# Optimization experiments

Measured on AMD Instinct MI355X. Metric: run time of the kernel, lower is better.

Reference implementation:

```python
import jax, jax.numpy as jnp
import numpy as np
import math

EPS = 1e-12


def _cmul(ar, ai, br, bi):
    return ar * br - ai * bi, ar * bi + ai * br


def _wilson_seed(x):
    # x: (B, 4, L, L) -> conj of canonical Wilson-line path, (B, L, L) re/im
    ux_r, ux_i, uy_r, uy_i = x[:, 0], x[:, 1], x[:, 2], x[:, 3]
    B, L, _ = ux_r.shape
    dt = x.dtype

    def step(c, u):
        cr, ci = c
        ur, ui = u
        nr, ni = _cmul(cr, ci, ur, ui)
        return (nr, ni), (nr, ni)

    # cumulative complex product along x at y=0
    init_r = jnp.ones((B,), dt)
    init_i = jnp.zeros((B,), dt)
    xs = (ux_r[:, :-1, 0].T, ux_i[:, :-1, 0].T)  # (L-1, B)
    _, (axr, axi) = jax.lax.scan(step, (init_r, init_i), xs)
    x_axis_r = jnp.concatenate([init_r[None], axr], 0).T  # (B, L)
    x_axis_i = jnp.concatenate([init_i[None], axi], 0).T

    # cumulative complex product along y, vectorized over x
    ys = (jnp.moveaxis(uy_r[:, :, :-1], 2, 0), jnp.moveaxis(uy_i[:, :, :-1], 2, 0))  # (L-1, B, L)
    _, (pr, pi_) = jax.lax.scan(step, (x_axis_r, x_axis_i), ys)
    path_r = jnp.moveaxis(jnp.concatenate([x_axis_r[None], pr], 0), 0, 2)  # (B, L, L)
    path_i = jnp.moveaxis(jnp.concatenate([x_axis_i[None], pi_], 0), 0, 2)
    return path_r, -path_i  # conjugate


def _wrap(t):
    return (t + math.pi) % (2.0 * math.pi) - math.pi


def _initial_features(x):
    seed_r, seed_i = _wilson_seed(x)
    ax = jnp.arctan2(x[:, 1], x[:, 0])
    ay = jnp.arctan2(x[:, 3], x[:, 2])
    plaq = _wrap(ax + jnp.roll(ay, -1, axis=1) - jnp.roll(ax, -1, axis=2) - ay)
    pc = jnp.cos(plaq)
    pavg = (pc + jnp.roll(pc, 1, 1) + jnp.roll(pc, -1, 1)
            + jnp.roll(pc, 1, 2) + jnp.roll(pc, -1, 2)) / 5.0
    scalars = jnp.stack([jnp.ones_like(pc), pc, pavg], axis=1)  # (B, 3, L, L)
    return seed_r[:, None] * scalars, seed_i[:, None] * scalars


def _transport_fwd(fr, fi, x, mu):
    lr, li = (x[:, 0], x[:, 1]) if mu == 0 else (x[:, 2], x[:, 3])
    sr = jnp.roll(fr, -1, axis=mu + 2)
    si = jnp.roll(fi, -1, axis=mu + 2)
    return _cmul(lr[:, None], li[:, None], sr, si)


def _transport_bwd(fr, fi, x, mu):
    lr, li = (x[:, 0], x[:, 1]) if mu == 0 else (x[:, 2], x[:, 3])
    cr = jnp.roll(lr, 1, axis=mu + 1)
    ci = jnp.roll(-li, 1, axis=mu + 1)
    sr = jnp.roll(fr, 1, axis=mu + 2)
    si = jnp.roll(fi, 1, axis=mu + 2)
    return _cmul(cr[:, None], ci[:, None], sr, si)


def _lconv(fr, fi, x, center, fwd_w, bwd_w):
    out_r = jnp.einsum('oi,bixy->boxy', center, fr)
    out_i = jnp.einsum('oi,bixy->boxy', center, fi)
    for mu in range(2):
        fr2, fi2 = _transport_fwd(fr, fi, x, mu)
        br2, bi2 = _transport_bwd(fr, fi, x, mu)
        out_r = out_r + jnp.einsum('oi,bixy->boxy', fwd_w[mu], fr2) \
                      + jnp.einsum('oi,bixy->boxy', bwd_w[mu], br2)
        out_i = out_i + jnp.einsum('oi,bixy->boxy', fwd_w[mu], fi2) \
                      + jnp.einsum('oi,bixy->boxy', bwd_w[mu], bi2)
    return out_r, out_i


def _modrelu(fr, fi, bias):
    mag = jnp.sqrt(fr * fr + fi * fi + EPS)
    act = jax.nn.relu(mag + bias[None, :, None, None])
    scale = act / jnp.maximum(mag, EPS)
    return fr * scale, fi * scale


def setup_inputs() -> dict:
    key = jax.random.key(0)
    ks = jax.random.split(key, 11)
    B, L, H, O = 64, 128, 16, 8
    s = 0.1
    return {
        'x': jax.random.normal(ks[0], (B, 4, L, L), jnp.float32),
        'center1': s * jax.random.normal(ks[1], (H, 3), jnp.float32),
        'fwd_w1': s * jax.random.normal(ks[2], (2, H, 3), jnp.float32),
        'bwd_w1': s * jax.random.normal(ks[3], (2, H, 3), jnp.float32),
        'bias1': jnp.zeros((H,), jnp.float32),
        'center2': s * jax.random.normal(ks[4], (O, H), jnp.float32),
        'fwd_w2': s * jax.random.normal(ks[5], (2, O, H), jnp.float32),
        'bwd_w2': s * jax.random.normal(ks[6], (2, O, H), jnp.float32),
        'bias2': jnp.zeros((O,), jnp.float32),
        'ro_weight': s * jax.random.normal(ks[7], (O,), jnp.float32),
        'ro_bias': jnp.zeros((1,), jnp.float32),
    }


def reference(x, center1, fwd_w1, bwd_w1, bias1, center2, fwd_w2, bwd_w2, bias2, ro_weight, ro_bias):
    fr, fi = _initial_features(x)
    fr, fi = _lconv(fr, fi, x, center1, fwd_w1, bwd_w1)
    fr, fi = _modrelu(fr, fi, bias1)
    fr, fi = _lconv(fr, fi, x, center2, fwd_w2, bwd_w2)
    fr, fi = _modrelu(fr, fi, bias2)
    inv = fr * fr + fi * fi
    return jnp.einsum('c,bcxy->bxy', ro_weight, inv)[:, None] + ro_bias.reshape(1, 1, 1, 1)
```

## Files before the change

### kernel.cpp

```cpp
#include <hip/hip_runtime.h>
#include <math.h>

#define LQ   128
#define BQ   64
#define LL   (LQ*LQ)
#define H1   16
#define O2   8
#define TILE 16
#define REG  18
#define NPTS (REG*REG)
#define PCR  22
#define PCN  (PCR*PCR)
#define LKR  23
#define LKN  (LKR*LKR)
#define SDR  20
#define SDN  (SDR*SDR)
#define FSTR 10

typedef float f2 __attribute__((ext_vector_type(2)));
using bf8 = __attribute__((ext_vector_type(8))) short;
using f4  = __attribute__((ext_vector_type(4))) float;

__device__ __forceinline__ int wrapi(int v) { return v & (LQ - 1); }

__device__ __forceinline__ unsigned pack_bf(float hi, float lo) {
    return __builtin_amdgcn_perm(__float_as_uint(hi), __float_as_uint(lo),
                                 0x07060302u);
}

#define WS_W1 ((size_t)BQ * LL)

__global__ __launch_bounds__(256)
void k_scan(const float* __restrict__ x,
            const float* __restrict__ c1, const float* __restrict__ fw1,
            const float* __restrict__ bw1, float* __restrict__ ws) {
    int blk = blockIdx.x;
    if (blk == BQ * 8) {
        int tid = threadIdx.x;
        if (tid < 120) {
            int t = tid / 24, r = tid - t * 24;
            int c = r >> 3, op = r & 7;
            const float* src = (t == 0) ? c1 : (t == 1) ? fw1 : (t == 2) ? bw1
                             : (t == 3) ? (fw1 + 48) : (bw1 + 48);
            float2 v = make_float2(src[(2 * op) * 3 + c], src[(2 * op + 1) * 3 + c]);
            ((float2*)ws)[WS_W1 + tid] = v;
        }
        return;
    }
    int b = blk >> 3, rq = blk & 7;
    int l = threadIdx.x & 63, w = threadIdx.x >> 6;
    const float* x0 = x + (size_t)b * 4 * LL;
    const float* x1 = x0 + LL;

    float ur0 = x0[(2 * l) * LQ],     ui0 = x1[(2 * l) * LQ];
    float ur1 = x0[(2 * l + 1) * LQ], ui1 = x1[(2 * l + 1) * LQ];
    float pr = ur0 * ur1 - ui0 * ui1;
    float pi = ur0 * ui1 + ui0 * ur1;
    for (int d = 1; d < 64; d <<= 1) {
        float qr = __shfl_up(pr, d, 64);
        float qi = __shfl_up(pi, d, 64);
        if (l >= d) {
            float nr = qr * pr - qi * pi;
            float ni = qr * pi + qi * pr;
            pr = nr; pi = ni;
        }
    }
    float er = __shfl_up(pr, 1, 64);
    float ei = __shfl_up(pi, 1, 64);
    if (l == 0) { er = 1.f; ei = 0.f; }
    float e1r = er * ur0 - ei * ui0;
    float e1i = er * ui0 + ei * ur0;

    const float* yrp = x + (size_t)(b * 4 + 2) * LL;
    const float* yip = yrp + LL;
    float4* seed4 = (float4*)ws;

    for (int k = 0; k < 4; ++k) {
        int i = rq * 16 + w * 4 + k;
        float cxr = __shfl((i & 1) ? e1r : er, i >> 1, 64);
        float cxi = __shfl((i & 1) ? e1i : ei, i >> 1, 64);
        const float* yr = yrp + (size_t)i * LQ;
        const float* yi = yip + (size_t)i * LQ;
        float vr0 = yr[2 * l],     vi0 = yi[2 * l];
        float vr1 = yr[2 * l + 1], vi1 = yi[2 * l + 1];
        float sr = vr0 * vr1 - vi0 * vi1;
        float si = vr0 * vi1 + vi0 * vr1;
        for (int d = 1; d < 64; d <<= 1) {
            float qr = __shfl_up(sr, d, 64);
            float qi = __shfl_up(si, d, 64);
            if (l >= d) {
                float nr = qr * sr - qi * si;
                float ni = qr * si + qi * sr;
                sr = nr; si = ni;
            }
        }
        float gr = __shfl_up(sr, 1, 64);
        float gi = __shfl_up(si, 1, 64);
        if (l == 0) { gr = 1.f; gi = 0.f; }
        float s0r = cxr * gr - cxi * gi;
        float s0i = cxr * gi + cxi * gr;
        float s1r = s0r * vr0 - s0i * vi0;
        float s1i = s0r * vi0 + s0i * vr0;
        seed4[((size_t)b * LL + (size_t)i * LQ) / 2 + l] =
            make_float4(s0r, -s0i, s1r, -s1i);
    }
}

__global__ __launch_bounds__(256, 4)
void k_main(const float* __restrict__ x,
            const float* __restrict__ c2, const float* __restrict__ fw2,
            const float* __restrict__ bw2, const float* __restrict__ b1,
            const float* __restrict__ b2,
            const float* __restrict__ ro, const float* __restrict__ rob,
            const float* __restrict__ ws, float* __restrict__ out) {
    __shared__ unsigned s_f1r[NPTS * FSTR];
    __shared__ unsigned s_f1i[NPTS * FSTR];
    __shared__ f2 s_ux[LKN];
    __shared__ f2 s_uy[LKN];
    __shared__ float s_pc[PCN];
    __shared__ f2 s_sd[SDN];
    int tid = threadIdx.x;
    int b = blockIdx.z, i0 = blockIdx.y * TILE, j0 = blockIdx.x * TILE;
    const float* x0 = x + (size_t)b * 4 * LL;
    const float* x1 = x0 + LL;
    const float* x2 = x0 + 2 * LL;
    const float* x3 = x0 + 3 * LL;
    const float2* seed = (const float2*)ws + (size_t)b * LL;
    const float2* W1 = (const float2*)ws + WS_W1;

    bool z1 = true;
#pragma unroll
    for (int h = 0; h < H1; ++h) z1 = z1 && (b1[h] == 0.f);
    bool z2 = true;
#pragma unroll
    for (int o = 0; o < O2; ++o) z2 = z2 && (b2[o] == 0.f);

    for (int p = tid; p < LKN; p += 256) {
        int ri = p / LKR, rj = p - ri * LKR;
        int gi = wrapi(i0 - 3 + ri), gj = wrapi(j0 - 3 + rj);
        int idx = gi * LQ + gj;
        s_ux[p] = (f2){x0[idx], x1[idx]};
        s_uy[p] = (f2){x2[idx], x3[idx]};
    }
    for (int p = tid; p < SDN; p += 256) {
        int ri = p / SDR, rj = p - ri * SDR;
        int gi = wrapi(i0 - 2 + ri), gj = wrapi(j0 - 2 + rj);
        float2 s = seed[gi * LQ + gj];
        s_sd[p] = (f2){s.x, s.y};
    }
    __syncthreads();

    for (int p = tid; p < PCN; p += 256) {
        int ri = p / PCR, rj = p - ri * PCR;
        int lb = ri * LKR + rj;
        f2 u1 = s_ux[lb];
        f2 u2 = s_uy[lb + LKR];
        f2 u3 = s_ux[lb + 1];
        f2 u4 = s_uy[lb];
        float ar = u1.x * u2.x - u1.y * u2.y, ai = u1.x * u2.y + u1.y * u2.x;
        float br = ar * u3.x + ai * u3.y,     bi = -ar * u3.y + ai * u3.x;
        float zr = br * u4.x + bi * u4.y,     zi = -br * u4.y + bi * u4.x;
        s_pc[p] = zr * __frsqrt_rn(fmaf(zr, zr, zi * zi) + 1e-30f);
    }
    __syncthreads();

#pragma unroll
    for (int pass = 0; pass < 2; ++pass) {
        int p = tid + pass * 256;
        if (pass == 1 && p >= NPTS) break;
        int ri = p / REG, rj = p - ri * REG;
        int sc = (ri + 1) * SDR + (rj + 1);
        int lb = (ri + 2) * LKR + (rj + 2);
        int cb = (ri + 2) * PCR + (rj + 2);

        f2 t[5]; float tc[5], tv[5];
        {
            f2 SC = s_sd[sc], SXP = s_sd[sc + SDR], SXM = s_sd[sc - SDR];
            f2 SYP = s_sd[sc + 1], SYM = s_sd[sc - 1];
            f2 lx = s_ux[lb], ly = s_uy[lb];
            f2 mx = s_ux[lb - LKR], my = s_uy[lb - 1];
            t[0] = SC;
            t[1] = (f2){lx.x * SXP.x - lx.y * SXP.y, lx.x * SXP.y + lx.y * SXP.x};
            t[2] = (f2){mx.x * SXM.x + mx.y * SXM.y, mx.x * SXM.y - mx.y * SXM.x};
            t[3] = (f2){ly.x * SYP.x - ly.y * SYP.y, ly.x * SYP.y + ly.y * SYP.x};
            t[4] = (f2){my.x * SYM.x + my.y * SYM.y, my.x * SYM.y - my.y * SYM.x};
            float p00 = s_pc[cb];
            float pP0 = s_pc[cb + PCR],     pM0 = s_pc[cb - PCR];
            float p0P = s_pc[cb + 1],       p0M = s_pc[cb - 1];
            float pP20 = s_pc[cb + 2*PCR],  pM20 = s_pc[cb - 2*PCR];
            float p0P2 = s_pc[cb + 2],      p0M2 = s_pc[cb - 2];
            float pPP = s_pc[cb + PCR + 1], pPM = s_pc[cb + PCR - 1];
            float pMP = s_pc[cb - PCR + 1], pMM = s_pc[cb - PCR - 1];
            tc[0] = p00; tc[1] = pP0; tc[2] = pM0; tc[3] = p0P; tc[4] = p0M;
            tv[0] = (p00 + pP0 + pM0 + p0P + p0M) * 0.2f;
            tv[1] = (pP0 + pP20 + p00 + pPP + pPM) * 0.2f;
            tv[2] = (pM0 + p00 + pM20 + pMP + pMM) * 0.2f;
            tv[3] = (p0P + pPP + pMP + p0P2 + p00) * 0.2f;
            tv[4] = (p0M + pPM + pMM + p00 + p0M2) * 0.2f;
        }

        f2 accr[8], acci[8];
#pragma unroll
        for (int op = 0; op < 8; ++op) { accr[op] = (f2){0.f, 0.f}; acci[op] = (f2){0.f, 0.f}; }
#pragma unroll
        for (int q = 0; q < 5; ++q) {
            f2 tcv = (f2){tc[q], tc[q]}, tvv = (f2){tv[q], tv[q]};
            f2 trv = (f2){t[q].x, t[q].x}, tiv = (f2){t[q].y, t[q].y};
            const float2* Wq = W1 + q * 24;
#pragma unroll
            for (int op = 0; op < 8; ++op) {
                float2 w0 = Wq[op], w1 = Wq[8 + op], w2 = Wq[16 + op];
                f2 mp = (f2){w0.x, w0.y};
                mp += (f2){w1.x, w1.y} * tcv;
                mp += (f2){w2.x, w2.y} * tvv;
                accr[op] += mp * trv;
                acci[op] += mp * tiv;
            }
        }
        if (!z1) {
#pragma unroll
            for (int op = 0; op < 8; ++op) {
                f2 q2 = accr[op] * accr[op] + acci[op] * acci[op] + (f2){1e-12f, 1e-12f};
                float s0 = fmaxf(fmaf(b1[2 * op],     __frsqrt_rn(q2.x), 1.f), 0.f);
                float s1 = fmaxf(fmaf(b1[2 * op + 1], __frsqrt_rn(q2.y), 1.f), 0.f);
                f2 sv = (f2){s0, s1};
                accr[op] *= sv; acci[op] *= sv;
            }
        }
        unsigned* fr_ = &s_f1r[p * FSTR];
        unsigned* fi_ = &s_f1i[p * FSTR];
#pragma unroll
        for (int d = 0; d < 4; ++d) {
            unsigned r0 = pack_bf(accr[2*d].y,   accr[2*d].x);
            unsigned r1 = pack_bf(accr[2*d+1].y, accr[2*d+1].x);
            unsigned q0 = pack_bf(acci[2*d].y,   acci[2*d].x);
            unsigned q1 = pack_bf(acci[2*d+1].y, acci[2*d+1].x);
            *(uint2*)&fr_[2*d] = make_uint2(r0, r1);
            *(uint2*)&fi_[2*d] = make_uint2(q0, q1);
        }
    }
    __syncthreads();

    int lane = tid & 63, w = tid >> 6;
    int quad = lane >> 4, nIdx = lane & 15;
    int half = quad >> 1;
    int koff = (quad & 1) * 4;

    const float* wLo[3] = {c2, bw2, bw2 + O2 * H1};
    const float* wHi[3] = {fw2, fw2 + O2 * H1, (const float*)0};
    bf8 afr[3];
#pragma unroll
    for (int pq = 0; pq < 3; ++pq) {
        bf8 z = {0, 0, 0, 0, 0, 0, 0, 0};
        const float* wsrc = half ? wHi[pq] : wLo[pq];
        int row = half ? (nIdx - 8) : nIdx;
        bool valid = half ? (nIdx >= 8 && wsrc != 0) : (nIdx < 8);
        if (valid) {
            const float* wp = wsrc + row * H1 + (quad & 1) * 8;
            float4 wa = *(const float4*)wp;
            float4 wb = *(const float4*)(wp + 4);
            uint4 u;
            u.x = pack_bf(wa.y, wa.x);
            u.y = pack_bf(wa.w, wa.z);
            u.z = pack_bf(wb.y, wb.x);
            u.w = pack_bf(wb.w, wb.z);
            __builtin_memcpy(&z, &u, 16);
        }
        afr[pq] = z;
    }
    float4 ro_lo = *(const float4*)ro;
    float4 ro_hi = *(const float4*)(ro + 4);
    float4 b2_lo = *(const float4*)b2;
    float4 b2_hi = *(const float4*)(b2 + 4);
    float4 zf4 = make_float4(0.f, 0.f, 0.f, 0.f);
    float4 rv = (quad == 0) ? ro_lo : ((quad == 1) ? ro_hi : zf4);
    float4 bv = (quad == 0) ? b2_lo : ((quad == 1) ? b2_hi : zf4);
    float rob0 = rob[0];

    for (int g = 0; g < 4; ++g) {
        int row = w * 4 + g;
        int posc = (row + 1) * REG + (nIdx + 1);
        int lb2 = (row + 3) * LKR + (nIdx + 3);
        f2 lx = s_ux[lb2], ly = s_uy[lb2];
        f2 mx = s_ux[lb2 - LKR], my = s_uy[lb2 - 1];

        float Lr[3], Li[3];
        Lr[0] = half ? lx.x : 1.f;   Li[0] = half ? lx.y : 0.f;
        Lr[1] = half ? ly.x : mx.x;  Li[1] = half ? ly.y : -mx.y;
        Lr[2] = half ? 0.f : my.x;   Li[2] = half ? 0.f : -my.y;
        int dpl[3];
        dpl[0] = half ? REG : 0;
        dpl[1] = half ? 1 : -REG;
        dpl[2] = -1;

        f4 a2r = {0.f, 0.f, 0.f, 0.f}, a2i = {0.f, 0.f, 0.f, 0.f};
#pragma unroll
        for (int pq = 0; pq < 3; ++pq) {
            int base = (posc + dpl[pq]) * FSTR + koff;
            uint2 rlo = *(const uint2*)&s_f1r[base];
            uint2 rhi = *(const uint2*)&s_f1r[base + 2];
            uint2 ilo = *(const uint2*)&s_f1i[base];
            uint2 ihi = *(const uint2*)&s_f1i[base + 2];
            bf8 br, bi;
            uint4 ur = {rlo.x, rlo.y, rhi.x, rhi.y};
            uint4 ui = {ilo.x, ilo.y, ihi.x, ihi.y};
            __builtin_memcpy(&br, &ur, 16);
            __builtin_memcpy(&bi, &ui, 16);
            f4 zc = {0.f, 0.f, 0.f, 0.f};
            f4 sr = __builtin_amdgcn_mfma_f32_16x16x32_bf16(afr[pq], br, zc, 0, 0, 0);
            f4 si = __builtin_amdgcn_mfma_f32_16x16x32_bf16(afr[pq], bi, zc, 0, 0, 0);
            a2r += Lr[pq] * sr - Li[pq] * si;
            a2i += Lr[pq] * si + Li[pq] * sr;
        }

#pragma unroll
        for (int c = 0; c < 4; ++c) {
            a2r[c] += __shfl_xor(a2r[c], 32, 64);
            a2i[c] += __shfl_xor(a2i[c], 32, 64);
        }

        f4 q4 = a2r * a2r + a2i * a2i;
        float res;
        if (z2) {
            res = rv.x * q4.x + rv.y * q4.y + rv.z * q4.z + rv.w * q4.w;
        } else {
            float bvv[4] = {bv.x, bv.y, bv.z, bv.w};
            float rvv[4] = {rv.x, rv.y, rv.z, rv.w};
            res = 0.f;
#pragma unroll
            for (int r = 0; r < 4; ++r) {
                float qq = q4[r];
                float s = fmaxf(fmaf(bvv[r], __frsqrt_rn(qq + 1e-12f), 1.f), 0.f);
                res = fmaf(rvv[r], s * s * qq, res);
            }
        }
        res += __shfl_xor(res, 16, 64);
        if (quad == 0)
            out[(size_t)b * LL + (size_t)(i0 + row) * LQ + (j0 + nIdx)] = res + rob0;
    }
}

extern "C" void kernel_launch(void* const* d_in, const int* in_sizes, int n_in,
                              void* d_out, int out_size, void* d_ws, size_t ws_size,
                              hipStream_t stream) {
    const float* x   = (const float*)d_in[0];
    const float* c1  = (const float*)d_in[1];
    const float* fw1 = (const float*)d_in[2];
    const float* bw1 = (const float*)d_in[3];
    const float* b1  = (const float*)d_in[4];
    const float* c2  = (const float*)d_in[5];
    const float* fw2 = (const float*)d_in[6];
    const float* bw2 = (const float*)d_in[7];
    const float* b2  = (const float*)d_in[8];
    const float* ro  = (const float*)d_in[9];
    const float* rob = (const float*)d_in[10];
    float* out = (float*)d_out;
    float* ws  = (float*)d_ws;

    k_scan<<<BQ * 8 + 1, 256, 0, stream>>>(x, c1, fw1, bw1, ws);
    dim3 grid(LQ / TILE, LQ / TILE, BQ);
    k_main<<<grid, 256, 0, stream>>>(x, c2, fw2, bw2, b1, b2,
                                     ro, rob, ws, out);
}
```

Measured before the change: 134.3 us.

## Precompute plaquette averages in LDS and split bf16 feature storage into uint4 arrays

Adds a shared-memory pass that computes the five-point plaquette average once per site, so the feature pass reads ten values per point instead of thirteen plus redundant sums. Splits the bf16 layer-1 feature buffer into separate lo/hi uint4 arrays, giving 128-bit stores and loads in place of strided uint2 accesses with padding. Layer-2 weights now use round-to-nearest-even bf16 conversion instead of truncation. The cost is an extra barrier and LDS array, and a change in weight rounding.

```diff
diff --git a/kernel.cpp b/kernel.cpp
--- a/kernel.cpp
+++ b/kernel.cpp
@@ -11,11 +11,12 @@
 #define NPTS (REG*REG)
 #define PCR  22
 #define PCN  (PCR*PCR)
+#define PVR  20
+#define PVN  (PVR*PVR)
 #define LKR  23
 #define LKN  (LKR*LKR)
 #define SDR  20
 #define SDN  (SDR*SDR)
-#define FSTR 10
 
 typedef float f2 __attribute__((ext_vector_type(2)));
 using bf8 = __attribute__((ext_vector_type(8))) short;
@@ -26,6 +27,11 @@
 __device__ __forceinline__ unsigned pack_bf(float hi, float lo) {
     return __builtin_amdgcn_perm(__float_as_uint(hi), __float_as_uint(lo),
                                  0x07060302u);
+}
+__device__ __forceinline__ unsigned bfrne(float f) {
+    unsigned u = __float_as_uint(f);
+    u += 0x7fffu + ((u >> 16) & 1u);
+    return u >> 16;
 }
 
 #define WS_W1 ((size_t)BQ * LL)
@@ -113,11 +119,14 @@
             const float* __restrict__ b2,
             const float* __restrict__ ro, const float* __restrict__ rob,
             const float* __restrict__ ws, float* __restrict__ out) {
-    __shared__ unsigned s_f1r[NPTS * FSTR];
-    __shared__ unsigned s_f1i[NPTS * FSTR];
+    __shared__ uint4 s_f1r_lo[NPTS];
+    __shared__ uint4 s_f1r_hi[NPTS];
+    __shared__ uint4 s_f1i_lo[NPTS];
+    __shared__ uint4 s_f1i_hi[NPTS];
     __shared__ f2 s_ux[LKN];
     __shared__ f2 s_uy[LKN];
     __shared__ float s_pc[PCN];
+    __shared__ float s_pv[PVN];
     __shared__ f2 s_sd[SDN];
     int tid = threadIdx.x;
     int b = blockIdx.z, i0 = blockIdx.y * TILE, j0 = blockIdx.x * TILE;
@@ -164,6 +173,14 @@
     }
     __syncthreads();
 
+    for (int p = tid; p < PVN; p += 256) {
+        int ri = p / PVR, rj = p - ri * PVR;
+        int c = (ri + 1) * PCR + (rj + 1);
+        s_pv[p] = (s_pc[c] + s_pc[c - PCR] + s_pc[c + PCR]
+                 + s_pc[c - 1] + s_pc[c + 1]) * 0.2f;
+    }
+    __syncthreads();
+
 #pragma unroll
     for (int pass = 0; pass < 2; ++pass) {
         int p = tid + pass * 256;
@@ -172,6 +189,7 @@
         int sc = (ri + 1) * SDR + (rj + 1);
         int lb = (ri + 2) * LKR + (rj + 2);
         int cb = (ri + 2) * PCR + (rj + 2);
+        int vb = (ri + 1) * PVR + (rj + 1);
 
         f2 t[5]; float tc[5], tv[5];
         {
@@ -184,19 +202,11 @@
             t[2] = (f2){mx.x * SXM.x + mx.y * SXM.y, mx.x * SXM.y - mx.y * SXM.x};
             t[3] = (f2){ly.x * SYP.x - ly.y * SYP.y, ly.x * SYP.y + ly.y * SYP.x};
             t[4] = (f2){my.x * SYM.x + my.y * SYM.y, my.x * SYM.y - my.y * SYM.x};
-            float p00 = s_pc[cb];
-            float pP0 = s_pc[cb + PCR],     pM0 = s_pc[cb - PCR];
-            float p0P = s_pc[cb + 1],       p0M = s_pc[cb - 1];
-            float pP20 = s_pc[cb + 2*PCR],  pM20 = s_pc[cb - 2*PCR];
-            float p0P2 = s_pc[cb + 2],      p0M2 = s_pc[cb - 2];
-            float pPP = s_pc[cb + PCR + 1], pPM = s_pc[cb + PCR - 1];
-            float pMP = s_pc[cb - PCR + 1], pMM = s_pc[cb - PCR - 1];
-            tc[0] = p00; tc[1] = pP0; tc[2] = pM0; tc[3] = p0P; tc[4] = p0M;
-            tv[0] = (p00 + pP0 + pM0 + p0P + p0M) * 0.2f;
-            tv[1] = (pP0 + pP20 + p00 + pPP + pPM) * 0.2f;
-            tv[2] = (pM0 + p00 + pM20 + pMP + pMM) * 0.2f;
-            tv[3] = (p0P + pPP + pMP + p0P2 + p00) * 0.2f;
-            tv[4] = (p0M + pPM + pMM + p00 + p0M2) * 0.2f;
+            tc[0] = s_pc[cb];       tv[0] = s_pv[vb];
+            tc[1] = s_pc[cb + PCR]; tv[1] = s_pv[vb + PVR];
+            tc[2] = s_pc[cb - PCR]; tv[2] = s_pv[vb - PVR];
+            tc[3] = s_pc[cb + 1];   tv[3] = s_pv[vb + 1];
+            tc[4] = s_pc[cb - 1];   tv[4] = s_pv[vb - 1];
         }
 
         f2 accr[8], acci[8];
@@ -227,24 +237,23 @@
                 accr[op] *= sv; acci[op] *= sv;
             }
         }
-        unsigned* fr_ = &s_f1r[p * FSTR];
-        unsigned* fi_ = &s_f1i[p * FSTR];
-#pragma unroll
-        for (int d = 0; d < 4; ++d) {
-            unsigned r0 = pack_bf(accr[2*d].y,   accr[2*d].x);
-            unsigned r1 = pack_bf(accr[2*d+1].y, accr[2*d+1].x);
-            unsigned q0 = pack_bf(acci[2*d].y,   acci[2*d].x);
-            unsigned q1 = pack_bf(acci[2*d+1].y, acci[2*d+1].x);
-            *(uint2*)&fr_[2*d] = make_uint2(r0, r1);
-            *(uint2*)&fi_[2*d] = make_uint2(q0, q1);
-        }
+        uint4 rlo, rhi, ilo, ihi;
+        rlo.x = pack_bf(accr[0].y, accr[0].x); rlo.y = pack_bf(accr[1].y, accr[1].x);
+        rlo.z = pack_bf(accr[2].y, accr[2].x); rlo.w = pack_bf(accr[3].y, accr[3].x);
+        rhi.x = pack_bf(accr[4].y, accr[4].x); rhi.y = pack_bf(accr[5].y, accr[5].x);
+        rhi.z = pack_bf(accr[6].y, accr[6].x); rhi.w = pack_bf(accr[7].y, accr[7].x);
+        ilo.x = pack_bf(acci[0].y, acci[0].x); ilo.y = pack_bf(acci[1].y, acci[1].x);
+        ilo.z = pack_bf(acci[2].y, acci[2].x); ilo.w = pack_bf(acci[3].y, acci[3].x);
+        ihi.x = pack_bf(acci[4].y, acci[4].x); ihi.y = pack_bf(acci[5].y, acci[5].x);
+        ihi.z = pack_bf(acci[6].y, acci[6].x); ihi.w = pack_bf(acci[7].y, acci[7].x);
+        s_f1r_lo[p] = rlo; s_f1r_hi[p] = rhi;
+        s_f1i_lo[p] = ilo; s_f1i_hi[p] = ihi;
     }
     __syncthreads();
 
     int lane = tid & 63, w = tid >> 6;
     int quad = lane >> 4, nIdx = lane & 15;
     int half = quad >> 1;
-    int koff = (quad & 1) * 4;
 
     const float* wLo[3] = {c2, bw2, bw2 + O2 * H1};
     const float* wHi[3] = {fw2, fw2 + O2 * H1, (const float*)0};
@@ -260,14 +269,17 @@
             float4 wa = *(const float4*)wp;
             float4 wb = *(const float4*)(wp + 4);
             uint4 u;
-            u.x = pack_bf(wa.y, wa.x);
-            u.y = pack_bf(wa.w, wa.z);
-            u.z = pack_bf(wb.y, wb.x);
-            u.w = pack_bf(wb.w, wb.z);
+            u.x = bfrne(wa.x) | (bfrne(wa.y) << 16);
+            u.y = bfrne(wa.z) | (bfrne(wa.w) << 16);
+            u.z = bfrne(wb.x) | (bfrne(wb.y) << 16);
+            u.w = bfrne(wb.z) | (bfrne(wb.w) << 16);
             __builtin_memcpy(&z, &u, 16);
         }
         afr[pq] = z;
     }
+    const uint4* rArr = (quad & 1) ? s_f1r_hi : s_f1r_lo;
+    const uint4* iArr = (quad & 1) ? s_f1i_hi : s_f1i_lo;
+
     float4 ro_lo = *(const float4*)ro;
     float4 ro_hi = *(const float4*)(ro + 4);
     float4 b2_lo = *(const float4*)b2;
@@ -296,14 +308,10 @@
         f4 a2r = {0.f, 0.f, 0.f, 0.f}, a2i = {0.f, 0.f, 0.f, 0.f};
 #pragma unroll
         for (int pq = 0; pq < 3; ++pq) {
-            int base = (posc + dpl[pq]) * FSTR + koff;
-            uint2 rlo = *(const uint2*)&s_f1r[base];
-            uint2 rhi = *(const uint2*)&s_f1r[base + 2];
-            uint2 ilo = *(const uint2*)&s_f1i[base];
-            uint2 ihi = *(const uint2*)&s_f1i[base + 2];
+            int pos = posc + dpl[pq];
+            uint4 ur = rArr[pos];
+            uint4 ui = iArr[pos];
             bf8 br, bi;
-            uint4 ur = {rlo.x, rlo.y, rhi.x, rhi.y};
-            uint4 ui = {ilo.x, ilo.y, ihi.x, ihi.y};
             __builtin_memcpy(&br, &ur, 16);
             __builtin_memcpy(&bi, &ui, 16);
             f4 zc = {0.f, 0.f, 0.f, 0.f};
```

Result: no change. 136.7 us (+1.8%).
